# Optimization experiments

Hardware: AMD Instinct MI355X
Metric: run time of the kernel (lower is better)

## Reference

```python
import jax, jax.numpy as jnp
import numpy as np

B, NFEAT, T, HID, LAT = 512, 512, 64, 1024, 2


def setup_inputs() -> dict:
    key = jax.random.key(0)
    ks = jax.random.split(key, 6)
    x = jax.random.normal(ks[0], (B, NFEAT, T), dtype=jnp.float32)
    We1 = jax.random.normal(ks[1], (NFEAT, HID), dtype=jnp.float32) / np.float32(np.sqrt(NFEAT))
    be1 = jnp.zeros((HID,), dtype=jnp.float32)
    We2 = jax.random.normal(ks[2], (HID, LAT), dtype=jnp.float32) / np.float32(np.sqrt(HID))
    be2 = jnp.zeros((LAT,), dtype=jnp.float32)
    Wd1 = jax.random.normal(ks[3], (LAT, HID), dtype=jnp.float32) / np.float32(np.sqrt(LAT))
    bd1 = jnp.zeros((HID,), dtype=jnp.float32)
    Wd2 = jax.random.normal(ks[4], (HID, NFEAT), dtype=jnp.float32) / np.float32(np.sqrt(HID))
    bd2 = jnp.zeros((NFEAT,), dtype=jnp.float32)
    return {"x": x, "We1": We1, "be1": be1, "We2": We2, "be2": be2,
            "Wd1": Wd1, "bd1": bd1, "Wd2": Wd2, "bd2": bd2}


def _autoencoder(x, We1, be1, We2, be2, Wd1, bd1, Wd2, bd2):
    # dense layers applied per timestep along the feature axis
    h = jnp.tanh(jnp.einsum('bnt,nh->bht', x, We1) + be1[None, :, None])
    y = jnp.einsum('bht,hl->blt', h, We2) + be2[None, :, None]          # (B, 2, T) latent
    hd = jnp.tanh(jnp.einsum('blt,lh->bht', y, Wd1) + bd1[None, :, None])
    x_ae = jnp.einsum('bht,hn->bnt', hd, Wd2) + bd2[None, :, None]      # (B, NFEAT, T)
    return y, x_ae


def _dmd(y):
    # windowing: (B, 2, T) -> (2B, T); interleaving rows == reshape
    yw = y.reshape(B * LAT, T)
    y_minus = yw[:, :-1]   # (2B, T-1)
    y_plus = yw[:, 1:]     # (2B, T-1)

    # linearity loss: || y_plus (I - V V^T) ||_F^2 (tf frobenius_norm = trace(M M^T))
    _, _, vh = jnp.linalg.svd(y_minus, full_matrices=False)  # vh: (T-1, T-1)
    V = vh.T
    proj = jnp.eye(T - 1, dtype=yw.dtype) - V @ V.T
    loss_mat = y_plus @ proj
    dmd_loss = jnp.sum(loss_mat * loss_mat)

    # DMD operator: Amat = X+ pinv(X-)
    Amat = y_plus @ jnp.linalg.pinv(y_minus)   # (2B, 2B)

    # y_pred[:, ii] = A^{ii+1} y0 (original overwrites column 0 with A y0)
    y0 = yw[:, 0]
    def step(Aexp, _):
        return Aexp @ Amat, Aexp @ y0
    _, preds = jax.lax.scan(step, Amat, None, length=T)   # (T, 2B)
    y_pred = preds.T.reshape(B, LAT, T)                    # undo windowing
    return dmd_loss, Amat, y_pred


def reference(x, We1, be1, We2, be2, Wd1, bd1, Wd2, bd2):
    y, x_ae = _autoencoder(x, We1, be1, We2, be2, Wd1, bd1, Wd2, bd2)
    dmd_loss, Amat, y_pred = _dmd(y)
    pred_loss = jnp.mean((y_pred - y) ** 2)               # mean MSE over last axis then batch
    ae_loss = jnp.mean((x[:, :, 0] - x_ae[:, :, 0]) ** 2)
    return (x_ae, y, dmd_loss, ae_loss, y_pred, Amat, pred_loss)
```

## Files before the change

kernel.cpp:

```cpp
#include <hip/hip_runtime.h>
#include <hip/hip_bf16.h>

#define Bz 512
#define NF 512
#define TT 64
#define HIDZ 1024
#define LATZ 2

static const size_t OFF_XAE   = 0;
static const size_t OFF_Y     = (size_t)Bz * NF * TT;
static const size_t OFF_DMD   = OFF_Y + (size_t)Bz * LATZ * TT;
static const size_t OFF_AE    = OFF_DMD + 1;
static const size_t OFF_YPRED = OFF_AE + 1;
static const size_t OFF_AMAT  = OFF_YPRED + (size_t)Bz * LATZ * TT;
static const size_t OFF_PRED  = OFF_AMAT + (size_t)1024 * 1024;

#define WS_G     0
#define WS_GINV  4096
#define WS_PROJ  8192
#define WS_P     16384
#define WS_YP    1179648
#define WS_W     1441792
#define WS_GP    1445888
#define WS_WP    1511424
#define WS_PP    1576960
#define WS_U     1642496
#define WS_WD2T  3538944
#define WS_WE1H  3801088
#define WS_WE1L  4063232

typedef __attribute__((ext_vector_type(8))) short bf16x8;
typedef __attribute__((ext_vector_type(4))) float f32x4;

__device__ __forceinline__ unsigned short f2bf(float f) {
  unsigned u = __float_as_uint(f);
  unsigned r = (u + 0x7fffu + ((u >> 16) & 1u)) >> 16;
  return (unsigned short)r;
}
__device__ __forceinline__ float bf2f(unsigned short h) {
  return __uint_as_float((unsigned)h << 16);
}
__device__ __forceinline__ uint4 pack8(const unsigned short* v) {
  return make_uint4((unsigned)v[0] | ((unsigned)v[1] << 16),
                    (unsigned)v[2] | ((unsigned)v[3] << 16),
                    (unsigned)v[4] | ((unsigned)v[5] << 16),
                    (unsigned)v[6] | ((unsigned)v[7] << 16));
}
__device__ __forceinline__ void split8(const float* v, bf16x8& hi, bf16x8& lo) {
#pragma unroll
  for (int e = 0; e < 8; ++e) {
    unsigned short h = f2bf(v[e]);
    hi[e] = (short)h;
    lo[e] = (short)f2bf(v[e] - bf2f(h));
  }
}

__device__ inline float blockReduceSum(float v) {
  __shared__ float sh[16];
  int lane = threadIdx.x & 63;
  int wid  = threadIdx.x >> 6;
#pragma unroll
  for (int off = 32; off > 0; off >>= 1) v += __shfl_down(v, off, 64);
  if (lane == 0) sh[wid] = v;
  __syncthreads();
  int nw = blockDim.x >> 6;
  v = (threadIdx.x < (unsigned)nw) ? sh[threadIdx.x] : 0.f;
  if (wid == 0) {
#pragma unroll
    for (int off = 8; off > 0; off >>= 1) v += __shfl_down(v, off, 64);
  }
  return v;
}

__global__ void k_init(float* dmd, float* ae, float* pred) {
  if (threadIdx.x == 0) { *dmd = 0.f; *ae = 0.f; *pred = 0.f; }
}

__global__ void k_we1t(const float* __restrict__ We1,
                       unsigned short* __restrict__ ah, unsigned short* __restrict__ al) {
  int s = blockIdx.x * 256 + threadIdx.x;
  int l = s & 63, mfg = (s >> 6) & 63, kt = s >> 12;
  int m = mfg * 16 + (l & 15);
  int k0 = kt * 32 + (l >> 4) * 8;
  unsigned short h[8], lo[8];
#pragma unroll
  for (int e = 0; e < 8; ++e) {
    float v = We1[(size_t)(k0 + e) * HIDZ + m];
    h[e] = f2bf(v);
    lo[e] = f2bf(v - bf2f(h[e]));
  }
  *(uint4*)(ah + (size_t)s * 8) = pack8(h);
  *(uint4*)(al + (size_t)s * 8) = pack8(lo);
}

__global__ __launch_bounds__(256, 2) void k_gemm1m(const float* __restrict__ x,
    const unsigned short* __restrict__ we1h, const unsigned short* __restrict__ we1l,
    const float* __restrict__ be1, const float* __restrict__ We2,
    float* __restrict__ ypartial) {
  __shared__ uint4 bh4[4][64], bl4[4][64];
  __shared__ float yredl[4][2][64];
  int o = blockIdx.x;
  int lbid = (o & 7) * 256 + (o >> 3);
  int b = lbid >> 2, hb = lbid & 3;
  int tid = threadIdx.x, w = tid >> 6, l = tid & 63, q = l >> 4, c = l & 15;
  const float* xb = x + (size_t)b * NF * TT;
  f32x4 acc[4][4];
#pragma unroll
  for (int i = 0; i < 4; ++i)
#pragma unroll
    for (int j = 0; j < 4; ++j) acc[i][j] = (f32x4)(0.f);
  for (int kt = 0; kt < 16; ++kt) {
    {
      const float* xp = xb + (size_t)(kt * 32 + q * 8) * TT + (w * 16 + c);
      float v[8];
#pragma unroll
      for (int e = 0; e < 8; ++e) v[e] = xp[e * TT];
      unsigned short h[8], lo[8];
#pragma unroll
      for (int e = 0; e < 8; ++e) {
        h[e] = f2bf(v[e]);
        lo[e] = f2bf(v[e] - bf2f(h[e]));
      }
      bh4[w][l] = pack8(h);
      bl4[w][l] = pack8(lo);
    }
    __syncthreads();
    bf16x8 ah[4], al[4], bhf[4], blf[4];
#pragma unroll
    for (int mf = 0; mf < 4; ++mf) {
      size_t slot = ((size_t)kt * 64 + hb * 16 + w * 4 + mf) * 64 + l;
      ah[mf] = *(const bf16x8*)(we1h + slot * 8);
      al[mf] = *(const bf16x8*)(we1l + slot * 8);
    }
#pragma unroll
    for (int nf = 0; nf < 4; ++nf) {
      bhf[nf] = *(bf16x8*)&bh4[nf][l];
      blf[nf] = *(bf16x8*)&bl4[nf][l];
    }
#pragma unroll
    for (int mf = 0; mf < 4; ++mf)
#pragma unroll
      for (int nf = 0; nf < 4; ++nf) {
        acc[mf][nf] = __builtin_amdgcn_mfma_f32_16x16x32_bf16(ah[mf], bhf[nf], acc[mf][nf], 0, 0, 0);
        acc[mf][nf] = __builtin_amdgcn_mfma_f32_16x16x32_bf16(ah[mf], blf[nf], acc[mf][nf], 0, 0, 0);
        acc[mf][nf] = __builtin_amdgcn_mfma_f32_16x16x32_bf16(al[mf], bhf[nf], acc[mf][nf], 0, 0, 0);
      }
    __syncthreads();
  }
  float p0[4] = {0.f, 0.f, 0.f, 0.f}, p1[4] = {0.f, 0.f, 0.f, 0.f};
#pragma unroll
  for (int mf = 0; mf < 4; ++mf) {
    int hbase = hb * 256 + w * 64 + mf * 16 + q * 4;
#pragma unroll
    for (int r = 0; r < 4; ++r) {
      int hh = hbase + r;
      float bias = be1[hh];
      float w20 = We2[2 * hh], w21 = We2[2 * hh + 1];
#pragma unroll
      for (int nf = 0; nf < 4; ++nf) {
        float hv = tanhf(acc[mf][nf][r] + bias);
        p0[nf] += hv * w20;
        p1[nf] += hv * w21;
      }
    }
  }
#pragma unroll
  for (int nf = 0; nf < 4; ++nf) {
    p0[nf] += __shfl_xor(p0[nf], 16, 64); p0[nf] += __shfl_xor(p0[nf], 32, 64);
    p1[nf] += __shfl_xor(p1[nf], 16, 64); p1[nf] += __shfl_xor(p1[nf], 32, 64);
  }
  if (q == 0) {
#pragma unroll
    for (int nf = 0; nf < 4; ++nf) {
      yredl[w][0][nf * 16 + c] = p0[nf];
      yredl[w][1][nf * 16 + c] = p1[nf];
    }
  }
  __syncthreads();
  if (tid < 128) {
    int lat = tid >> 6, t = tid & 63;
    float s = yredl[0][lat][t] + yredl[1][lat][t] + yredl[2][lat][t] + yredl[3][lat][t];
    ypartial[(((size_t)hb * Bz + b) * LATZ + lat) * TT + t] = s;
  }
}

__global__ void k_yred(const float* __restrict__ yp, const float* __restrict__ be2,
                       float* __restrict__ y) {
  int idx = blockIdx.x * 256 + threadIdx.x;
  int t = idx & 63, l = (idx >> 6) & 1, b = idx >> 7;
  float s = be2[l];
#pragma unroll
  for (int hb = 0; hb < 4; ++hb) s += yp[(((size_t)hb * Bz + b) * LATZ + l) * TT + t];
  y[idx] = s;
}

__global__ void k_wd2t(const float* __restrict__ Wd2, unsigned short* __restrict__ at) {
  int s = blockIdx.x * 256 + threadIdx.x;
  int l = s & 63;
  int frag = s >> 6;
  int mf = frag & 31, kt = frag >> 5;
  int n = mf * 16 + (l & 15);
  int kbase = kt * 32 + (l >> 4) * 8;
  unsigned short v[8];
#pragma unroll
  for (int e = 0; e < 8; ++e) v[e] = f2bf(Wd2[(size_t)(kbase + e) * NF + n]);
  *(uint4*)(at + (size_t)s * 8) = pack8(v);
}

__device__ __forceinline__ void stage_hd(int kt, unsigned short* dst, int q,
                                         float y0t, float y1t,
                                         const float* __restrict__ Wd1,
                                         const float* __restrict__ bd1) {
  int k = kt * 32 + q * 8;
  float4 w0a = *(const float4*)&Wd1[k];
  float4 w0b = *(const float4*)&Wd1[k + 4];
  float4 w1a = *(const float4*)&Wd1[HIDZ + k];
  float4 w1b = *(const float4*)&Wd1[HIDZ + k + 4];
  float4 ba  = *(const float4*)&bd1[k];
  float4 bb  = *(const float4*)&bd1[k + 4];
  float h[8];
  h[0] = tanhf(y0t * w0a.x + y1t * w1a.x + ba.x);
  h[1] = tanhf(y0t * w0a.y + y1t * w1a.y + ba.y);
  h[2] = tanhf(y0t * w0a.z + y1t * w1a.z + ba.z);
  h[3] = tanhf(y0t * w0a.w + y1t * w1a.w + ba.w);
  h[4] = tanhf(y0t * w0b.x + y1t * w1b.x + bb.x);
  h[5] = tanhf(y0t * w0b.y + y1t * w1b.y + bb.y);
  h[6] = tanhf(y0t * w0b.z + y1t * w1b.z + bb.z);
  h[7] = tanhf(y0t * w0b.w + y1t * w1b.w + bb.w);
  unsigned short hv[8];
#pragma unroll
  for (int e = 0; e < 8; ++e) hv[e] = f2bf(h[e]);
  *(uint4*)dst = pack8(hv);
}

__global__ __launch_bounds__(256, 2) void k_gemm4m(const float* __restrict__ y,
                                                   const float* __restrict__ Wd1,
                                                   const float* __restrict__ bd1,
                                                   const unsigned short* __restrict__ at,
                                                   const float* __restrict__ bd2,
                                                   float* __restrict__ xae) {
  __shared__ __align__(16) unsigned short bbuf[2][4][64][8];
  __shared__ float ys[2][64];
  int b = blockIdx.x, tid = threadIdx.x;
  int w = tid >> 6, l = tid & 63;
  int c = l & 15, q = l >> 4;
  if (tid < 128) ys[tid >> 6][tid & 63] = y[((size_t)b * LATZ + (tid >> 6)) * TT + (tid & 63)];
  __syncthreads();
  int t_s = w * 16 + c;
  float y0t = ys[0][t_s], y1t = ys[1][t_s];
  f32x4 acc[8][4];
#pragma unroll
  for (int i = 0; i < 8; ++i)
#pragma unroll
    for (int j = 0; j < 4; ++j) acc[i][j] = (f32x4)(0.f);
  const bf16x8* A = (const bf16x8*)at;
  stage_hd(0, &bbuf[0][w][l][0], q, y0t, y1t, Wd1, bd1);
  for (int kt = 0; kt < 32; ++kt) {
    __syncthreads();
    if (kt + 1 < 32) stage_hd(kt + 1, &bbuf[(kt + 1) & 1][w][l][0], q, y0t, y1t, Wd1, bd1);
    bf16x8 bf[4];
#pragma unroll
    for (int t2 = 0; t2 < 4; ++t2) bf[t2] = *(const bf16x8*)&bbuf[kt & 1][t2][l][0];
    bf16x8 af[8];
#pragma unroll
    for (int mf = 0; mf < 8; ++mf) af[mf] = A[(size_t)((kt * 32 + w * 8 + mf) * 64) + l];
#pragma unroll
    for (int mf = 0; mf < 8; ++mf)
#pragma unroll
      for (int t2 = 0; t2 < 4; ++t2)
        acc[mf][t2] = __builtin_amdgcn_mfma_f32_16x16x32_bf16(af[mf], bf[t2], acc[mf][t2], 0, 0, 0);
  }
#pragma unroll
  for (int mf = 0; mf < 8; ++mf) {
    int nb = w * 128 + mf * 16 + q * 4;
#pragma unroll
    for (int r = 0; r < 4; ++r) {
      int n = nb + r;
      float bias = bd2[n];
#pragma unroll
      for (int t2 = 0; t2 < 4; ++t2)
        xae[((size_t)b * NF + n) * TT + t2 * 16 + c] = acc[mf][t2][r] + bias;
    }
  }
}

__global__ __launch_bounds__(256) void k_Gall(const float* __restrict__ y,
                                              float* __restrict__ Gp, float* __restrict__ Wp) {
  __shared__ float ys[64][65];
  int cb = blockIdx.x, tid = threadIdx.x;
#pragma unroll
  for (int p = 0; p < 16; ++p) {
    int f = tid + p * 256;
    int rr = f >> 6, cc = f & 63;
    ys[rr][cc] = y[(size_t)(cb * 64 + rr) * 64 + cc];
  }
  __syncthreads();
#pragma unroll
  for (int p = 0; p < 16; ++p) {
    int o = tid + p * 256;
    if (o < 3969) {
      int i = o / 63, j = o % 63;
      float gs = 0.f, wsv = 0.f;
#pragma unroll
      for (int rr = 0; rr < 64; ++rr) {
        float yi = ys[rr][i];
        gs  += yi * ys[rr][j];
        wsv += yi * ys[rr][j + 1];
      }
      Gp[cb * 3969 + o] = gs;
      Wp[cb * 3969 + o] = wsv;
    }
  }
}

__global__ void k_Gred(const float* __restrict__ Gp, const float* __restrict__ Wp,
                       float* __restrict__ G, float* __restrict__ W) {
  int idx = blockIdx.x * 256 + threadIdx.x;
  if (idx >= 2 * 3969) return;
  int sel = idx >= 3969;
  int o = idx - sel * 3969;
  const float* src = sel ? Wp : Gp;
  float s = 0.f;
#pragma unroll
  for (int cb = 0; cb < 16; ++cb) s += src[cb * 3969 + o];
  (sel ? W : G)[o] = s;
}

__global__ __launch_bounds__(64, 1) void k_inv(const float* __restrict__ G,
                                               float* __restrict__ Ginv) {
  int i = threadIdx.x;
  float a[126];
  if (i < 63) {
#pragma unroll
    for (int j = 0; j < 63; ++j) a[j] = G[i * 63 + j];
  } else {
#pragma unroll
    for (int j = 0; j < 63; ++j) a[j] = (j == 0) ? 1.f : 0.f;
  }
#pragma unroll
  for (int j = 0; j < 63; ++j) a[63 + j] = (i == j) ? 1.f : 0.f;
#pragma unroll
  for (int k = 0; k < 63; ++k) {
    float pivot = __shfl(a[k], k, 64);
    float rp = 1.f / pivot;
    float m = a[k];
    bool isk = (i == k);
#pragma unroll
    for (int j = k; j < 126; ++j) {
      float t = __shfl(a[j], k, 64) * rp;
      a[j] = isk ? t : (a[j] - m * t);
    }
  }
  if (i < 63) {
#pragma unroll
    for (int j = 0; j < 63; ++j) Ginv[i * 63 + j] = a[63 + j];
  }
}

__global__ __launch_bounds__(256) void k_P(const float* __restrict__ y,
                                           const float* __restrict__ Ginv,
                                           float* __restrict__ P) {
  __shared__ float ys[64][65];
  int r0 = blockIdx.x * 64, tid = threadIdx.x;
#pragma unroll
  for (int p = 0; p < 16; ++p) {
    int f = tid + p * 256;
    ys[f >> 6][f & 63] = y[(size_t)(r0 + (f >> 6)) * 64 + (f & 63)];
  }
  __syncthreads();
#pragma unroll
  for (int p = 0; p < 16; ++p) {
    int o = tid + p * 256;
    if (o < 4032) {
      int i = o >> 6, rr = o & 63;
      float s = 0.f;
#pragma unroll
      for (int j = 0; j < 63; ++j) s += Ginv[i * 63 + j] * ys[rr][j];
      P[(size_t)i * 1024 + r0 + rr] = s;
    }
  }
}

__global__ __launch_bounds__(256) void k_projc(const float* __restrict__ y,
                                               const float* __restrict__ P,
                                               float* __restrict__ Pp) {
  __shared__ float ps[63][64];
  __shared__ float ysm[64][65];
  int cb = blockIdx.x, tid = threadIdx.x;
#pragma unroll
  for (int p = 0; p < 16; ++p) {
    int f = tid + p * 256;
    if (f < 4032) {
      int i = f >> 6, rr = f & 63;
      ps[i][rr] = P[(size_t)i * 1024 + cb * 64 + rr];
    }
    int rr2 = f >> 6, cc = f & 63;
    ysm[rr2][cc] = y[(size_t)(cb * 64 + rr2) * 64 + cc];
  }
  __syncthreads();
#pragma unroll
  for (int p = 0; p < 16; ++p) {
    int o = tid + p * 256;
    if (o < 3969) {
      int i = o / 63, j = o % 63;
      float s = 0.f;
#pragma unroll
      for (int rr = 0; rr < 64; ++rr) s += ps[i][rr] * ysm[rr][j];
      Pp[cb * 3969 + o] = s;
    }
  }
}

__global__ void k_projred(const float* __restrict__ Pp, float* __restrict__ proj) {
  int o = blockIdx.x * 256 + threadIdx.x;
  if (o >= 3969) return;
  int i = o / 63, j = o % 63;
  float s = 0.f;
#pragma unroll
  for (int cb = 0; cb < 16; ++cb) s += Pp[cb * 3969 + o];
  proj[o] = ((i == j) ? 1.f : 0.f) - s;
}

__global__ __launch_bounds__(256) void k_Amat(const float* __restrict__ y,
                                              const float* __restrict__ P,
                                              float* __restrict__ amat_out) {
  __shared__ float Yp[64][65];
  __shared__ float Ps[63][64];
  int r0 = blockIdx.x * 64, p0 = blockIdx.y * 64;
  int tid = threadIdx.x, tx = tid & 15, ty = tid >> 4;
#pragma unroll
  for (int p = 0; p < 16; ++p) {
    int f = tid + p * 256;
    Yp[f >> 6][f & 63] = y[(size_t)(p0 + (f >> 6)) * 64 + (f & 63)];
  }
#pragma unroll
  for (int p = 0; p < 16; ++p) {
    int f = tid + p * 256;
    if (f < 4032) {
      int j = f >> 6, rr = f & 63;
      Ps[j][rr] = P[(size_t)j * 1024 + r0 + rr];
    }
  }
  __syncthreads();
  float acc[4][4] = {};
  for (int j = 0; j < 63; ++j) {
    float a0 = Yp[ty * 4 + 0][j + 1];
    float a1 = Yp[ty * 4 + 1][j + 1];
    float a2 = Yp[ty * 4 + 2][j + 1];
    float a3 = Yp[ty * 4 + 3][j + 1];
    float4 bv = *(float4*)&Ps[j][tx * 4];
    acc[0][0] += a0 * bv.x; acc[0][1] += a0 * bv.y; acc[0][2] += a0 * bv.z; acc[0][3] += a0 * bv.w;
    acc[1][0] += a1 * bv.x; acc[1][1] += a1 * bv.y; acc[1][2] += a1 * bv.z; acc[1][3] += a1 * bv.w;
    acc[2][0] += a2 * bv.x; acc[2][1] += a2 * bv.y; acc[2][2] += a2 * bv.z; acc[2][3] += a2 * bv.w;
    acc[3][0] += a3 * bv.x; acc[3][1] += a3 * bv.y; acc[3][2] += a3 * bv.z; acc[3][3] += a3 * bv.w;
  }
#pragma unroll
  for (int i = 0; i < 4; ++i) {
#pragma unroll
    for (int jj = 0; jj < 4; ++jj) {
      size_t idx = (size_t)(p0 + ty * 4 + i) * 1024 + r0 + tx * 4 + jj;
      amat_out[idx] = acc[i][jj];
    }
  }
}

__global__ __launch_bounds__(256) void k_dmdloss(const float* __restrict__ y,
                                                 const float* __restrict__ proj,
                                                 float* __restrict__ out_dmd) {
  __shared__ float ps[3969];
  int tid = threadIdx.x;
  for (int f = tid; f < 3969; f += 256) ps[f] = proj[f];
  __syncthreads();
  int p = blockIdx.x * 256 + tid;
  float yp[63];
#pragma unroll
  for (int k = 0; k < 63; ++k) yp[k] = y[(size_t)p * 64 + k + 1];
  float accv = 0.f;
  for (int j = 0; j < 63; ++j) {
    float s = 0.f;
#pragma unroll
    for (int k = 0; k < 63; ++k) s += yp[k] * ps[k * 63 + j];
    accv += s * s;
  }
  float tot = blockReduceSum(accv);
  if (tid == 0) atomicAdd(out_dmd, tot);
}

__global__ __launch_bounds__(64, 1) void k_chain(const float* __restrict__ G,
                                                 const float* __restrict__ W,
                                                 const float* __restrict__ Ginv,
                                                 float* __restrict__ U) {
  __shared__ float wl[63][64];
  __shared__ float zl[64];
  __shared__ float ul[64];
  int i = threadIdx.x;
  float g[63];
  if (i < 63) {
#pragma unroll
    for (int k = 0; k < 63; ++k) g[k] = Ginv[i * 63 + k];
    for (int k = 0; k < 63; ++k) wl[k][i] = W[k * 63 + i];
    zl[i] = G[i * 63];
  } else {
#pragma unroll
    for (int k = 0; k < 63; ++k) g[k] = 0.f;
  }
  __syncthreads();
  float m[63];
#pragma unroll
  for (int j = 0; j < 63; ++j) {
    float s = 0.f;
#pragma unroll
    for (int k = 0; k < 63; ++k) s += g[k] * wl[k][j];
    m[j] = s;
  }
  float u = 0.f;
#pragma unroll
  for (int k = 0; k < 63; ++k) u += g[k] * zl[k];
  for (int t = 0; t < 64; ++t) {
    if (i < 63) U[t * 64 + i] = u;
    ul[i] = u;
    __syncthreads();
    float un = 0.f;
#pragma unroll
    for (int j = 0; j < 63; ++j) un += m[j] * ul[j];
    __syncthreads();
    u = un;
  }
}

__global__ __launch_bounds__(256) void k_ypred(const float* __restrict__ y,
                                               const float* __restrict__ U,
                                               float* __restrict__ ypred) {
  __shared__ float yp[64][65];
  __shared__ float ul[64][65];
  int rb = blockIdx.x, tid = threadIdx.x;
#pragma unroll
  for (int p = 0; p < 16; ++p) {
    int f = tid + p * 256;
    int a = f >> 6, b2 = f & 63;
    yp[a][b2] = y[(size_t)(rb * 64 + a) * 64 + b2];
    ul[a][b2] = U[a * 64 + b2];
  }
  __syncthreads();
  int rr = tid >> 2, tg = tid & 3;
  float acc[16] = {};
  for (int j = 0; j < 63; ++j) {
    float yv = yp[rr][j + 1];
#pragma unroll
    for (int tt = 0; tt < 16; ++tt) acc[tt] += yv * ul[tg * 16 + tt][j];
  }
  float* op = ypred + (size_t)(rb * 64 + rr) * 64 + tg * 16;
#pragma unroll
  for (int e = 0; e < 8; ++e)
    *(float2*)&op[e * 2] = make_float2(acc[2 * e], acc[2 * e + 1]);
}

__global__ __launch_bounds__(256) void k_predloss(const float* __restrict__ y,
                                                  const float* __restrict__ ypred,
                                                  float* __restrict__ outp) {
  int i = blockIdx.x * 256 + threadIdx.x;
  float d = ypred[i] - y[i];
  float tot = blockReduceSum(d * d);
  if (threadIdx.x == 0) atomicAdd(outp, tot * (1.f / 65536.f));
}

__global__ __launch_bounds__(256) void k_aeloss(const float* __restrict__ x,
                                                const float* __restrict__ xae,
                                                float* __restrict__ outp) {
  int i = blockIdx.x * 256 + threadIdx.x;
  float d = x[(size_t)i * 64] - xae[(size_t)i * 64];
  float tot = blockReduceSum(d * d);
  if (threadIdx.x == 0) atomicAdd(outp, tot * (1.f / 262144.f));
}

extern "C" void kernel_launch(void* const* d_in, const int* in_sizes, int n_in,
                              void* d_out, int out_size, void* d_ws, size_t ws_size,
                              hipStream_t stream) {
  (void)in_sizes; (void)n_in; (void)out_size; (void)ws_size;
  const float* x   = (const float*)d_in[0];
  const float* We1 = (const float*)d_in[1];
  const float* be1 = (const float*)d_in[2];
  const float* We2 = (const float*)d_in[3];
  const float* be2 = (const float*)d_in[4];
  const float* Wd1 = (const float*)d_in[5];
  const float* bd1 = (const float*)d_in[6];
  const float* Wd2 = (const float*)d_in[7];
  const float* bd2 = (const float*)d_in[8];
  float* out = (float*)d_out;
  float* wsf = (float*)d_ws;

  float* y_out = out + OFF_Y;
  unsigned short* wd2t = (unsigned short*)(wsf + WS_WD2T);
  unsigned short* we1h = (unsigned short*)(wsf + WS_WE1H);
  unsigned short* we1l = (unsigned short*)(wsf + WS_WE1L);

  k_init<<<1, 64, 0, stream>>>(out + OFF_DMD, out + OFF_AE, out + OFF_PRED);
  k_we1t<<<256, 256, 0, stream>>>(We1, we1h, we1l);
  k_wd2t<<<256, 256, 0, stream>>>(Wd2, wd2t);
  k_gemm1m<<<2048, 256, 0, stream>>>(x, we1h, we1l, be1, We2, wsf + WS_YP);
  k_yred<<<256, 256, 0, stream>>>(wsf + WS_YP, be2, y_out);
  k_gemm4m<<<512, 256, 0, stream>>>(y_out, Wd1, bd1, wd2t, bd2, out + OFF_XAE);
  k_Gall<<<16, 256, 0, stream>>>(y_out, wsf + WS_GP, wsf + WS_WP);
  k_Gred<<<32, 256, 0, stream>>>(wsf + WS_GP, wsf + WS_WP, wsf + WS_G, wsf + WS_W);
  k_inv<<<1, 64, 0, stream>>>(wsf + WS_G, wsf + WS_GINV);
  k_chain<<<1, 64, 0, stream>>>(wsf + WS_G, wsf + WS_W, wsf + WS_GINV, wsf + WS_U);
  k_P<<<16, 256, 0, stream>>>(y_out, wsf + WS_GINV, wsf + WS_P);
  k_projc<<<16, 256, 0, stream>>>(y_out, wsf + WS_P, wsf + WS_PP);
  k_projred<<<16, 256, 0, stream>>>(wsf + WS_PP, wsf + WS_PROJ);
  k_Amat<<<dim3(16, 16), 256, 0, stream>>>(y_out, wsf + WS_P, out + OFF_AMAT);
  k_dmdloss<<<4, 256, 0, stream>>>(y_out, wsf + WS_PROJ, out + OFF_DMD);
  k_ypred<<<16, 256, 0, stream>>>(y_out, wsf + WS_U, out + OFF_YPRED);
  k_predloss<<<256, 256, 0, stream>>>(y_out, out + OFF_YPRED, out + OFF_PRED);
  k_aeloss<<<1024, 256, 0, stream>>>(x, out + OFF_XAE, out + OFF_AE);
}
```

Baseline: 612.6 us.

## Fuse small kernels and restructure first GEMM to full-hidden blocks with double buffering

Merges the init and weight-conversion kernels into one prep kernel. The first GEMM now uses 512-thread blocks that cover all 1024 hidden units per batch, which removes the partial-y workspace and its reduction kernel, and it double-buffers the x staging in LDS. Several tail kernels are also merged: inverse with chain, P with projection, ypred with pred loss, and the ae loss folded into the decoder GEMM. The goal is fewer launches and less global round-tripping, at the cost of fewer, larger blocks in GEMM1 (512 instead of 2048) and higher register pressure.

```diff
diff --git a/kernel.cpp b/kernel.cpp
--- a/kernel.cpp
+++ b/kernel.cpp
@@ -19,7 +19,6 @@
 #define WS_GINV  4096
 #define WS_PROJ  8192
 #define WS_P     16384
-#define WS_YP    1179648
 #define WS_W     1441792
 #define WS_GP    1445888
 #define WS_WP    1511424
@@ -46,14 +45,6 @@
                     (unsigned)v[4] | ((unsigned)v[5] << 16),
                     (unsigned)v[6] | ((unsigned)v[7] << 16));
 }
-__device__ __forceinline__ void split8(const float* v, bf16x8& hi, bf16x8& lo) {
-#pragma unroll
-  for (int e = 0; e < 8; ++e) {
-    unsigned short h = f2bf(v[e]);
-    hi[e] = (short)h;
-    lo[e] = (short)f2bf(v[e] - bf2f(h));
-  }
-}
 
 __device__ inline float blockReduceSum(float v) {
   __shared__ float sh[16];
@@ -72,85 +63,111 @@
   return v;
 }
 
-__global__ void k_init(float* dmd, float* ae, float* pred) {
-  if (threadIdx.x == 0) { *dmd = 0.f; *ae = 0.f; *pred = 0.f; }
-}
-
-__global__ void k_we1t(const float* __restrict__ We1,
-                       unsigned short* __restrict__ ah, unsigned short* __restrict__ al) {
-  int s = blockIdx.x * 256 + threadIdx.x;
-  int l = s & 63, mfg = (s >> 6) & 63, kt = s >> 12;
-  int m = mfg * 16 + (l & 15);
-  int k0 = kt * 32 + (l >> 4) * 8;
-  unsigned short h[8], lo[8];
-#pragma unroll
-  for (int e = 0; e < 8; ++e) {
-    float v = We1[(size_t)(k0 + e) * HIDZ + m];
-    h[e] = f2bf(v);
-    lo[e] = f2bf(v - bf2f(h[e]));
-  }
-  *(uint4*)(ah + (size_t)s * 8) = pack8(h);
-  *(uint4*)(al + (size_t)s * 8) = pack8(lo);
-}
-
-__global__ __launch_bounds__(256, 2) void k_gemm1m(const float* __restrict__ x,
+__global__ void k_prep(const float* __restrict__ We1,
+                       unsigned short* __restrict__ ah, unsigned short* __restrict__ al,
+                       const float* __restrict__ Wd2, unsigned short* __restrict__ at,
+                       float* dmd, float* ae, float* pred) {
+  int bid = blockIdx.x, tid = threadIdx.x;
+  if (bid < 256) {
+    int s = bid * 256 + tid;
+    int l = s & 63, mfg = (s >> 6) & 63, kt = s >> 12;
+    int m = mfg * 16 + (l & 15);
+    int k0 = kt * 32 + (l >> 4) * 8;
+    unsigned short h[8], lo[8];
+#pragma unroll
+    for (int e = 0; e < 8; ++e) {
+      float v = We1[(size_t)(k0 + e) * HIDZ + m];
+      h[e] = f2bf(v);
+      lo[e] = f2bf(v - bf2f(h[e]));
+    }
+    *(uint4*)(ah + (size_t)s * 8) = pack8(h);
+    *(uint4*)(al + (size_t)s * 8) = pack8(lo);
+  } else if (bid < 512) {
+    int s = (bid - 256) * 256 + tid;
+    int l = s & 63;
+    int frag = s >> 6;
+    int mf = frag & 31, kt = frag >> 5;
+    int n = mf * 16 + (l & 15);
+    int kbase = kt * 32 + (l >> 4) * 8;
+    unsigned short v[8];
+#pragma unroll
+    for (int e = 0; e < 8; ++e) v[e] = f2bf(Wd2[(size_t)(kbase + e) * NF + n]);
+    *(uint4*)(at + (size_t)s * 8) = pack8(v);
+  } else if (tid == 0) {
+    *dmd = 0.f; *ae = 0.f; *pred = 0.f;
+  }
+}
+
+__device__ __forceinline__ void stage_x(const float* __restrict__ xb, int kt,
+                                        int nf_s, int ls, int half8,
+                                        uint2* dh, uint2* dl) {
+  int k0 = kt * 32 + (ls >> 4) * 8 + half8 * 4;
+  int t_s = nf_s * 16 + (ls & 15);
+  const float* xp = xb + (size_t)k0 * TT + t_s;
+  float v[4];
+#pragma unroll
+  for (int e = 0; e < 4; ++e) v[e] = xp[e * TT];
+  unsigned short h[4], lo[4];
+#pragma unroll
+  for (int e = 0; e < 4; ++e) {
+    h[e] = f2bf(v[e]);
+    lo[e] = f2bf(v[e] - bf2f(h[e]));
+  }
+  *dh = make_uint2((unsigned)h[0] | ((unsigned)h[1] << 16),
+                   (unsigned)h[2] | ((unsigned)h[3] << 16));
+  *dl = make_uint2((unsigned)lo[0] | ((unsigned)lo[1] << 16),
+                   (unsigned)lo[2] | ((unsigned)lo[3] << 16));
+}
+
+__global__ __launch_bounds__(512, 2) void k_gemm1m(const float* __restrict__ x,
     const unsigned short* __restrict__ we1h, const unsigned short* __restrict__ we1l,
     const float* __restrict__ be1, const float* __restrict__ We2,
-    float* __restrict__ ypartial) {
-  __shared__ uint4 bh4[4][64], bl4[4][64];
-  __shared__ float yredl[4][2][64];
-  int o = blockIdx.x;
-  int lbid = (o & 7) * 256 + (o >> 3);
-  int b = lbid >> 2, hb = lbid & 3;
+    const float* __restrict__ be2, float* __restrict__ y) {
+  __shared__ __align__(16) uint4 bh4[2][4][64], bl4[2][4][64];
+  __shared__ float yredl[8][2][64];
+  int b = blockIdx.x;
   int tid = threadIdx.x, w = tid >> 6, l = tid & 63, q = l >> 4, c = l & 15;
   const float* xb = x + (size_t)b * NF * TT;
-  f32x4 acc[4][4];
-#pragma unroll
-  for (int i = 0; i < 4; ++i)
+  int half8 = tid >> 8;
+  int rest = tid & 255;
+  int nf_s = rest >> 6, ls = rest & 63;
+  f32x4 acc[8][4];
+#pragma unroll
+  for (int i = 0; i < 8; ++i)
 #pragma unroll
     for (int j = 0; j < 4; ++j) acc[i][j] = (f32x4)(0.f);
+  stage_x(xb, 0, nf_s, ls, half8, (uint2*)&bh4[0][nf_s][ls] + half8,
+          (uint2*)&bl4[0][nf_s][ls] + half8);
+  __syncthreads();
   for (int kt = 0; kt < 16; ++kt) {
-    {
-      const float* xp = xb + (size_t)(kt * 32 + q * 8) * TT + (w * 16 + c);
-      float v[8];
-#pragma unroll
-      for (int e = 0; e < 8; ++e) v[e] = xp[e * TT];
-      unsigned short h[8], lo[8];
-#pragma unroll
-      for (int e = 0; e < 8; ++e) {
-        h[e] = f2bf(v[e]);
-        lo[e] = f2bf(v[e] - bf2f(h[e]));
+    int cur = kt & 1;
+    if (kt + 1 < 16)
+      stage_x(xb, kt + 1, nf_s, ls, half8, (uint2*)&bh4[cur ^ 1][nf_s][ls] + half8,
+              (uint2*)&bl4[cur ^ 1][nf_s][ls] + half8);
+    bf16x8 bhf[4], blf[4];
+#pragma unroll
+    for (int nf = 0; nf < 4; ++nf) {
+      bhf[nf] = *(bf16x8*)&bh4[cur][nf][l];
+      blf[nf] = *(bf16x8*)&bl4[cur][nf][l];
+    }
+#pragma unroll
+    for (int mf = 0; mf < 8; ++mf) {
+      size_t slot = ((size_t)kt * 64 + w * 8 + mf) * 64 + l;
+      bf16x8 ah = *(const bf16x8*)(we1h + slot * 8);
+      bf16x8 al = *(const bf16x8*)(we1l + slot * 8);
+#pragma unroll
+      for (int nf = 0; nf < 4; ++nf) {
+        acc[mf][nf] = __builtin_amdgcn_mfma_f32_16x16x32_bf16(ah, bhf[nf], acc[mf][nf], 0, 0, 0);
+        acc[mf][nf] = __builtin_amdgcn_mfma_f32_16x16x32_bf16(ah, blf[nf], acc[mf][nf], 0, 0, 0);
+        acc[mf][nf] = __builtin_amdgcn_mfma_f32_16x16x32_bf16(al, bhf[nf], acc[mf][nf], 0, 0, 0);
       }
-      bh4[w][l] = pack8(h);
-      bl4[w][l] = pack8(lo);
     }
     __syncthreads();
-    bf16x8 ah[4], al[4], bhf[4], blf[4];
-#pragma unroll
-    for (int mf = 0; mf < 4; ++mf) {
-      size_t slot = ((size_t)kt * 64 + hb * 16 + w * 4 + mf) * 64 + l;
-      ah[mf] = *(const bf16x8*)(we1h + slot * 8);
-      al[mf] = *(const bf16x8*)(we1l + slot * 8);
-    }
-#pragma unroll
-    for (int nf = 0; nf < 4; ++nf) {
-      bhf[nf] = *(bf16x8*)&bh4[nf][l];
-      blf[nf] = *(bf16x8*)&bl4[nf][l];
-    }
-#pragma unroll
-    for (int mf = 0; mf < 4; ++mf)
-#pragma unroll
-      for (int nf = 0; nf < 4; ++nf) {
-        acc[mf][nf] = __builtin_amdgcn_mfma_f32_16x16x32_bf16(ah[mf], bhf[nf], acc[mf][nf], 0, 0, 0);
-        acc[mf][nf] = __builtin_amdgcn_mfma_f32_16x16x32_bf16(ah[mf], blf[nf], acc[mf][nf], 0, 0, 0);
-        acc[mf][nf] = __builtin_amdgcn_mfma_f32_16x16x32_bf16(al[mf], bhf[nf], acc[mf][nf], 0, 0, 0);
-      }
-    __syncthreads();
   }
   float p0[4] = {0.f, 0.f, 0.f, 0.f}, p1[4] = {0.f, 0.f, 0.f, 0.f};
 #pragma unroll
-  for (int mf = 0; mf < 4; ++mf) {
-    int hbase = hb * 256 + w * 64 + mf * 16 + q * 4;
+  for (int mf = 0; mf < 8; ++mf) {
+    int hbase = w * 128 + mf * 16 + q * 4;
 #pragma unroll
     for (int r = 0; r < 4; ++r) {
       int hh = hbase + r;
@@ -179,32 +196,11 @@
   __syncthreads();
   if (tid < 128) {
     int lat = tid >> 6, t = tid & 63;
-    float s = yredl[0][lat][t] + yredl[1][lat][t] + yredl[2][lat][t] + yredl[3][lat][t];
-    ypartial[(((size_t)hb * Bz + b) * LATZ + lat) * TT + t] = s;
-  }
-}
-
-__global__ void k_yred(const float* __restrict__ yp, const float* __restrict__ be2,
-                       float* __restrict__ y) {
-  int idx = blockIdx.x * 256 + threadIdx.x;
-  int t = idx & 63, l = (idx >> 6) & 1, b = idx >> 7;
-  float s = be2[l];
-#pragma unroll
-  for (int hb = 0; hb < 4; ++hb) s += yp[(((size_t)hb * Bz + b) * LATZ + l) * TT + t];
-  y[idx] = s;
-}
-
-__global__ void k_wd2t(const float* __restrict__ Wd2, unsigned short* __restrict__ at) {
-  int s = blockIdx.x * 256 + threadIdx.x;
-  int l = s & 63;
-  int frag = s >> 6;
-  int mf = frag & 31, kt = frag >> 5;
-  int n = mf * 16 + (l & 15);
-  int kbase = kt * 32 + (l >> 4) * 8;
-  unsigned short v[8];
-#pragma unroll
-  for (int e = 0; e < 8; ++e) v[e] = f2bf(Wd2[(size_t)(kbase + e) * NF + n]);
-  *(uint4*)(at + (size_t)s * 8) = pack8(v);
+    float s = be2[lat];
+#pragma unroll
+    for (int ww = 0; ww < 8; ++ww) s += yredl[ww][lat][t];
+    y[((size_t)b * LATZ + lat) * TT + t] = s;
+  }
 }
 
 __device__ __forceinline__ void stage_hd(int kt, unsigned short* dst, int q,
@@ -238,7 +234,9 @@
                                                    const float* __restrict__ bd1,
                                                    const unsigned short* __restrict__ at,
                                                    const float* __restrict__ bd2,
-                                                   float* __restrict__ xae) {
+                                                   const float* __restrict__ x,
+                                                   float* __restrict__ xae,
+                                                   float* __restrict__ ae_out) {
   __shared__ __align__(16) unsigned short bbuf[2][4][64][8];
   __shared__ float ys[2][64];
   int b = blockIdx.x, tid = threadIdx.x;
@@ -282,6 +280,20 @@
         xae[((size_t)b * NF + n) * TT + t2 * 16 + c] = acc[mf][t2][r] + bias;
     }
   }
+  float aeacc = 0.f;
+  if (c == 0) {
+#pragma unroll
+    for (int mf = 0; mf < 8; ++mf) {
+#pragma unroll
+      for (int r = 0; r < 4; ++r) {
+        int n = w * 128 + mf * 16 + q * 4 + r;
+        float d = x[((size_t)b * NF + n) * TT] - (acc[mf][0][r] + bd2[n]);
+        aeacc += d * d;
+      }
+    }
+  }
+  float tot = blockReduceSum(aeacc);
+  if (tid == 0) atomicAdd(ae_out, tot * (1.f / 262144.f));
 }
 
 __global__ __launch_bounds__(256) void k_Gall(const float* __restrict__ y,
@@ -326,8 +338,13 @@
   (sel ? W : G)[o] = s;
 }
 
-__global__ __launch_bounds__(64, 1) void k_inv(const float* __restrict__ G,
-                                               float* __restrict__ Ginv) {
+__global__ __launch_bounds__(64, 1) void k_invchain(const float* __restrict__ G,
+                                                    const float* __restrict__ W,
+                                                    float* __restrict__ Ginv,
+                                                    float* __restrict__ U) {
+  __shared__ float wl[63][64];
+  __shared__ float zl[64];
+  __shared__ float ul[64];
   int i = threadIdx.x;
   float a[126];
   if (i < 63) {
@@ -354,18 +371,44 @@
   if (i < 63) {
 #pragma unroll
     for (int j = 0; j < 63; ++j) Ginv[i * 63 + j] = a[63 + j];
-  }
-}
-
-__global__ __launch_bounds__(256) void k_P(const float* __restrict__ y,
-                                           const float* __restrict__ Ginv,
-                                           float* __restrict__ P) {
+    for (int k = 0; k < 63; ++k) wl[k][i] = W[k * 63 + i];
+    zl[i] = G[i * 63];
+  }
+  __syncthreads();
+  float m[63];
+#pragma unroll
+  for (int j = 0; j < 63; ++j) {
+    float s = 0.f;
+#pragma unroll
+    for (int k = 0; k < 63; ++k) s += a[63 + k] * wl[k][j];
+    m[j] = s;
+  }
+  float u = 0.f;
+#pragma unroll
+  for (int k = 0; k < 63; ++k) u += a[63 + k] * zl[k];
+  for (int t = 0; t < 64; ++t) {
+    if (i < 63) U[t * 64 + i] = u;
+    ul[i] = (i < 63) ? u : 0.f;
+    __syncthreads();
+    float un = 0.f;
+#pragma unroll
+    for (int j = 0; j < 63; ++j) un += m[j] * ul[j];
+    __syncthreads();
+    u = un;
+  }
+}
+
+__global__ __launch_bounds__(256) void k_Pprojc(const float* __restrict__ y,
+                                                const float* __restrict__ Ginv,
+                                                float* __restrict__ P,
+                                                float* __restrict__ Pp) {
   __shared__ float ys[64][65];
-  int r0 = blockIdx.x * 64, tid = threadIdx.x;
+  __shared__ float ps[63][64];
+  int cb = blockIdx.x, tid = threadIdx.x;
 #pragma unroll
   for (int p = 0; p < 16; ++p) {
     int f = tid + p * 256;
-    ys[f >> 6][f & 63] = y[(size_t)(r0 + (f >> 6)) * 64 + (f & 63)];
+    ys[f >> 6][f & 63] = y[(size_t)(cb * 64 + (f >> 6)) * 64 + (f & 63)];
   }
   __syncthreads();
 #pragma unroll
@@ -373,29 +416,14 @@
     int o = tid + p * 256;
     if (o < 4032) {
       int i = o >> 6, rr = o & 63;
-      float s = 0.f;
-#pragma unroll
-      for (int j = 0; j < 63; ++j) s += Ginv[i * 63 + j] * ys[rr][j];
-      P[(size_t)i * 1024 + r0 + rr] = s;
-    }
-  }
-}
-
-__global__ __launch_bounds__(256) void k_projc(const float* __restrict__ y,
-                                               const float* __restrict__ P,
-                                               float* __restrict__ Pp) {
-  __shared__ float ps[63][64];
-  __shared__ float ysm[64][65];
-  int cb = blockIdx.x, tid = threadIdx.x;
-#pragma unroll
-  for (int p = 0; p < 16; ++p) {
-    int f = tid + p * 256;
-    if (f < 4032) {
-      int i = f >> 6, rr = f & 63;
-      ps[i][rr] = P[(size_t)i * 1024 + cb * 64 + rr];
-    }
-    int rr2 = f >> 6, cc = f & 63;
-    ysm[rr2][cc] = y[(size_t)(cb * 64 + rr2) * 64 + cc];
+      if (i < 63) {
+        float s = 0.f;
+#pragma unroll
+        for (int j = 0; j < 63; ++j) s += Ginv[i * 63 + j] * ys[rr][j];
+        ps[i][rr] = s;
+        P[(size_t)i * 1024 + cb * 64 + rr] = s;
+      }
+    }
   }
   __syncthreads();
 #pragma unroll
@@ -405,7 +433,7 @@
       int i = o / 63, j = o % 63;
       float s = 0.f;
 #pragma unroll
-      for (int rr = 0; rr < 64; ++rr) s += ps[i][rr] * ysm[rr][j];
+      for (int rr = 0; rr < 64; ++rr) s += ps[i][rr] * ys[rr][j];
       Pp[cb * 3969 + o] = s;
     }
   }
@@ -486,51 +514,10 @@
   if (tid == 0) atomicAdd(out_dmd, tot);
 }
 
-__global__ __launch_bounds__(64, 1) void k_chain(const float* __restrict__ G,
-                                                 const float* __restrict__ W,
-                                                 const float* __restrict__ Ginv,
-                                                 float* __restrict__ U) {
-  __shared__ float wl[63][64];
-  __shared__ float zl[64];
-  __shared__ float ul[64];
-  int i = threadIdx.x;
-  float g[63];
-  if (i < 63) {
-#pragma unroll
-    for (int k = 0; k < 63; ++k) g[k] = Ginv[i * 63 + k];
-    for (int k = 0; k < 63; ++k) wl[k][i] = W[k * 63 + i];
-    zl[i] = G[i * 63];
-  } else {
-#pragma unroll
-    for (int k = 0; k < 63; ++k) g[k] = 0.f;
-  }
-  __syncthreads();
-  float m[63];
-#pragma unroll
-  for (int j = 0; j < 63; ++j) {
-    float s = 0.f;
-#pragma unroll
-    for (int k = 0; k < 63; ++k) s += g[k] * wl[k][j];
-    m[j] = s;
-  }
-  float u = 0.f;
-#pragma unroll
-  for (int k = 0; k < 63; ++k) u += g[k] * zl[k];
-  for (int t = 0; t < 64; ++t) {
-    if (i < 63) U[t * 64 + i] = u;
-    ul[i] = u;
-    __syncthreads();
-    float un = 0.f;
-#pragma unroll
-    for (int j = 0; j < 63; ++j) un += m[j] * ul[j];
-    __syncthreads();
-    u = un;
-  }
-}
-
-__global__ __launch_bounds__(256) void k_ypred(const float* __restrict__ y,
-                                               const float* __restrict__ U,
-                                               float* __restrict__ ypred) {
+__global__ __launch_bounds__(256) void k_ypredloss(const float* __restrict__ y,
+                                                   const float* __restrict__ U,
+                                                   float* __restrict__ ypred,
+                                                   float* __restrict__ pred_out) {
   __shared__ float yp[64][65];
   __shared__ float ul[64][65];
   int rb = blockIdx.x, tid = threadIdx.x;
@@ -550,27 +537,17 @@
     for (int tt = 0; tt < 16; ++tt) acc[tt] += yv * ul[tg * 16 + tt][j];
   }
   float* op = ypred + (size_t)(rb * 64 + rr) * 64 + tg * 16;
+  float se = 0.f;
+#pragma unroll
+  for (int tt = 0; tt < 16; ++tt) {
+    float d = acc[tt] - yp[rr][tg * 16 + tt];
+    se += d * d;
+  }
 #pragma unroll
   for (int e = 0; e < 8; ++e)
     *(float2*)&op[e * 2] = make_float2(acc[2 * e], acc[2 * e + 1]);
-}
-
-__global__ __launch_bounds__(256) void k_predloss(const float* __restrict__ y,
-                                                  const float* __restrict__ ypred,
-                                                  float* __restrict__ outp) {
-  int i = blockIdx.x * 256 + threadIdx.x;
-  float d = ypred[i] - y[i];
-  float tot = blockReduceSum(d * d);
-  if (threadIdx.x == 0) atomicAdd(outp, tot * (1.f / 65536.f));
-}
-
-__global__ __launch_bounds__(256) void k_aeloss(const float* __restrict__ x,
-                                                const float* __restrict__ xae,
-                                                float* __restrict__ outp) {
-  int i = blockIdx.x * 256 + threadIdx.x;
-  float d = x[(size_t)i * 64] - xae[(size_t)i * 64];
-  float tot = blockReduceSum(d * d);
-  if (threadIdx.x == 0) atomicAdd(outp, tot * (1.f / 262144.f));
+  float tot = blockReduceSum(se);
+  if (tid == 0) atomicAdd(pred_out, tot * (1.f / 65536.f));
 }
 
 extern "C" void kernel_launch(void* const* d_in, const int* in_sizes, int n_in,
@@ -594,22 +571,17 @@
   unsigned short* we1h = (unsigned short*)(wsf + WS_WE1H);
   unsigned short* we1l = (unsigned short*)(wsf + WS_WE1L);
 
-  k_init<<<1, 64, 0, stream>>>(out + OFF_DMD, out + OFF_AE, out + OFF_PRED);
-  k_we1t<<<256, 256, 0, stream>>>(We1, we1h, we1l);
-  k_wd2t<<<256, 256, 0, stream>>>(Wd2, wd2t);
-  k_gemm1m<<<2048, 256, 0, stream>>>(x, we1h, we1l, be1, We2, wsf + WS_YP);
-  k_yred<<<256, 256, 0, stream>>>(wsf + WS_YP, be2, y_out);
-  k_gemm4m<<<512, 256, 0, stream>>>(y_out, Wd1, bd1, wd2t, bd2, out + OFF_XAE);
+  k_prep<<<513, 256, 0, stream>>>(We1, we1h, we1l, Wd2, wd2t,
+                                  out + OFF_DMD, out + OFF_AE, out + OFF_PRED);
+  k_gemm1m<<<512, 512, 0, stream>>>(x, we1h, we1l, be1, We2, be2, y_out);
+  k_gemm4m<<<512, 256, 0, stream>>>(y_out, Wd1, bd1, wd2t, bd2, x,
+                                    out + OFF_XAE, out + OFF_AE);
   k_Gall<<<16, 256, 0, stream>>>(y_out, wsf + WS_GP, wsf + WS_WP);
   k_Gred<<<32, 256, 0, stream>>>(wsf + WS_GP, wsf + WS_WP, wsf + WS_G, wsf + WS_W);
-  k_inv<<<1, 64, 0, stream>>>(wsf + WS_G, wsf + WS_GINV);
-  k_chain<<<1, 64, 0, stream>>>(wsf + WS_G, wsf + WS_W, wsf + WS_GINV, wsf + WS_U);
-  k_P<<<16, 256, 0, stream>>>(y_out, wsf + WS_GINV, wsf + WS_P);
-  k_projc<<<16, 256, 0, stream>>>(y_out, wsf + WS_P, wsf + WS_PP);
+  k_invchain<<<1, 64, 0, stream>>>(wsf + WS_G, wsf + WS_W, wsf + WS_GINV, wsf + WS_U);
+  k_Pprojc<<<16, 256, 0, stream>>>(y_out, wsf + WS_GINV, wsf + WS_P, wsf + WS_PP);
   k_projred<<<16, 256, 0, stream>>>(wsf + WS_PP, wsf + WS_PROJ);
   k_Amat<<<dim3(16, 16), 256, 0, stream>>>(y_out, wsf + WS_P, out + OFF_AMAT);
   k_dmdloss<<<4, 256, 0, stream>>>(y_out, wsf + WS_PROJ, out + OFF_DMD);
-  k_ypred<<<16, 256, 0, stream>>>(y_out, wsf + WS_U, out + OFF_YPRED);
-  k_predloss<<<256, 256, 0, stream>>>(y_out, out + OFF_YPRED, out + OFF_PRED);
-  k_aeloss<<<1024, 256, 0, stream>>>(x, out + OFF_XAE, out + OFF_AE);
-}
+  k_ypredloss<<<16, 256, 0, stream>>>(y_out, wsf + WS_U, out + OFF_YPRED, out + OFF_PRED);
+}
```

Result: slower. 650.9 us (+6.2%).
